# Optimization experiments

Measured on AMD Instinct MI355X. Metric: run time of the kernel, lower is better.

The kernel has to match this reference:

```python
import jax, jax.numpy as jnp
import numpy as np

B, T, D, H = 4, 2048, 1024, 16
HD = D // H


def setup_inputs() -> dict:
    key = jax.random.key(0)
    ks = jax.random.split(key, 9)
    s = 1.0 / np.sqrt(D)
    return {
        "x": jax.random.normal(ks[0], (B, T, D), dtype=jnp.float32),
        "Wq": jax.random.normal(ks[1], (D, D), dtype=jnp.float32) * s,
        "bq": jnp.zeros((D,), dtype=jnp.float32),
        "Wk": jax.random.normal(ks[2], (D, D), dtype=jnp.float32) * s,
        "bk": jnp.zeros((D,), dtype=jnp.float32),
        "Wv": jax.random.normal(ks[3], (D, D), dtype=jnp.float32) * s,
        "bv": jnp.zeros((D,), dtype=jnp.float32),
        "Wo": jax.random.normal(ks[4], (D, D), dtype=jnp.float32) * s,
        "bo": jnp.zeros((D,), dtype=jnp.float32),
    }


def reference(x, Wq, bq, Wk, bk, Wv, bv, Wo, bo):
    b, t, c = x.shape
    h, hd = H, HD
    scale = hd ** -0.5
    # projections: [B,T,C] -> [B,H,T,hd]
    q = (x @ Wq.T + bq).reshape(b, t, h, hd).transpose(0, 2, 1, 3)
    k = (x @ Wk.T + bk).reshape(b, t, h, hd).transpose(0, 2, 1, 3)
    v = (x @ Wv.T + bv).reshape(b, t, h, hd).transpose(0, 2, 1, 3)
    # scores [B,H,T,T], causal mask (no kv cache path, T > 1)
    attn = jnp.einsum("bhqd,bhkd->bhqk", q, k) * scale
    causal = jnp.triu(jnp.ones((t, t), dtype=bool), k=1)
    attn = jnp.where(causal, -jnp.inf, attn)
    attn = jax.nn.softmax(attn, axis=-1)
    out = jnp.einsum("bhqk,bhkd->bhqd", attn, v)
    out = out.transpose(0, 2, 1, 3).reshape(b, t, c)
    return (out @ Wo.T + bo, k, v)
```

## Files before the change

### kernel.cpp

```cpp
#include <hip/hip_runtime.h>
#include <hip/hip_bf16.h>
#include <cstdint>


typedef short bf16x8 __attribute__((ext_vector_type(8)));
typedef float f32x4 __attribute__((ext_vector_type(4)));

#define GLDS16(g, l)                                                          \
  __builtin_amdgcn_global_load_lds(                                           \
      (const __attribute__((address_space(1))) void*)(g),                     \
      (__attribute__((address_space(3))) void*)(l), 16, 0, 0)

static __device__ __forceinline__ short f2b(float f) {
  union { float f; unsigned u; } x; x.f = f;
  unsigned r = (x.u + 0x7FFFu + ((x.u >> 16) & 1u)) >> 16;
  return (short)r;
}

static __device__ __forceinline__ unsigned cvtpk2(float a, float b) {
  unsigned r;
  asm("v_cvt_pk_bf16_f32 %0, %1, %2" : "=v"(r) : "v"(a), "v"(b));
  return r;
}

__global__ void cvt_f32_bf16(const float* __restrict__ src, short* __restrict__ dst, int n4) {
  int i = blockIdx.x * blockDim.x + threadIdx.x;
  if (i < n4) {
    float4 v = ((const float4*)src)[i];
    short4 o; o.x = f2b(v.x); o.y = f2b(v.y); o.z = f2b(v.z); o.w = f2b(v.w);
    ((short4*)dst)[i] = o;
  }
}

__global__ void cvt_w4(const float* __restrict__ a, const float* __restrict__ b,
                       const float* __restrict__ c, const float* __restrict__ d,
                       short* __restrict__ dst) {
  int i = blockIdx.x * blockDim.x + threadIdx.x;
  int sel = i >> 18, j = i & 262143;
  const float* src = sel == 0 ? a : sel == 1 ? b : sel == 2 ? c : d;
  float4 v = ((const float4*)src)[j];
  short4 o; o.x = f2b(v.x); o.y = f2b(v.y); o.z = f2b(v.z); o.w = f2b(v.w);
  ((short4*)dst)[i] = o;
}

#define PIPE_STEP(BUF)                                                        \
  {                                                                          \
    asm volatile("s_waitcnt vmcnt(4) lgkmcnt(0)" ::: "memory");              \
    __builtin_amdgcn_s_barrier();                                            \
    __builtin_amdgcn_sched_barrier(0);                                       \
    stage((((BUF) + 2) % 3), (tile + 2) * 32);                               \
    compute(BUF);                                                            \
    ++tile;                                                                  \
  }

#define PIPE_TAIL()                                                          \
  asm volatile("s_waitcnt vmcnt(4) lgkmcnt(0)" ::: "memory");                \
  __builtin_amdgcn_s_barrier();                                              \
  __builtin_amdgcn_sched_barrier(0);                                         \
  compute(0);                                                   \
  asm volatile("s_waitcnt vmcnt(0) lgkmcnt(0)" ::: "memory");                \
  __builtin_amdgcn_s_barrier();                                              \
  __builtin_amdgcn_sched_barrier(0);                                         \
  compute(1);

__global__ __launch_bounds__(256) void gemm_qkv(
    const short* __restrict__ A,
    const short* __restrict__ W0, const short* __restrict__ W1, const short* __restrict__ W2,
    const float* __restrict__ b0, const float* __restrict__ b1, const float* __restrict__ b2,
    float* __restrict__ kf, float* __restrict__ vf,
    short* __restrict__ qbo, short* __restrict__ kbo, short* __restrict__ vtbo) {
  __shared__ short SM[24576];
  const int t = threadIdx.x;
  const int lane = t & 63;
  const int w = t >> 6;
  const int wm = w >> 1, wn = w & 1;
  const int quad = lane >> 4, l15 = lane & 15;
  const int bm = blockIdx.y;
  const int sel = blockIdx.x >> 3, bn = blockIdx.x & 7;
  const short* Bm = sel == 0 ? W0 : (sel == 1 ? W1 : W2);
  const float* bias = sel == 0 ? b0 : (sel == 1 ? b1 : b2);

  f32x4 acc[4][4];
  for (int i = 0; i < 4; i++)
    for (int j = 0; j < 4; j++) acc[i][j] = (f32x4){0.f, 0.f, 0.f, 0.f};

  const int c0 = t, c1 = t + 256;
  const int r0 = c0 >> 2, cc0 = c0 & 3;
  const int r1 = c1 >> 2, cc1 = c1 & 3;
  const short* Abase = A + (size_t)bm * 128 * 1024;
  const short* Bbase = Bm + (size_t)bn * 128 * 1024;

  auto stage = [&](int buf, int kk) {
    short* A_ = SM + buf * 4096;
    short* B_ = SM + 12288 + buf * 4096;
    GLDS16(Abase + (size_t)r0 * 1024 + kk + cc0 * 8, A_ + c0 * 8);
    GLDS16(Abase + (size_t)r1 * 1024 + kk + cc1 * 8, A_ + c1 * 8);
    GLDS16(Bbase + (size_t)r0 * 1024 + kk + cc0 * 8, B_ + c0 * 8);
    GLDS16(Bbase + (size_t)r1 * 1024 + kk + cc1 * 8, B_ + c1 * 8);
  };
  auto compute = [&](int buf) {
    const short* A_ = SM + buf * 4096;
    const short* B_ = SM + 12288 + buf * 4096;
    bf16x8 af[4], bfr[4];
    for (int mt = 0; mt < 4; mt++)
      af[mt] = *(const bf16x8*)(A_ + (wm * 64 + mt * 16 + l15) * 32 + quad * 8);
    for (int nt = 0; nt < 4; nt++)
      bfr[nt] = *(const bf16x8*)(B_ + (wn * 64 + nt * 16 + l15) * 32 + quad * 8);
    for (int mt = 0; mt < 4; mt++)
      for (int nt = 0; nt < 4; nt++)
        acc[mt][nt] = __builtin_amdgcn_mfma_f32_16x16x32_bf16(af[mt], bfr[nt], acc[mt][nt], 0, 0, 0);
  };

  stage(0, 0);
  stage(1, 32);
  int tile = 0;
  for (int ii = 0; ii < 10; ++ii) {
    PIPE_STEP(0) PIPE_STEP(1) PIPE_STEP(2)
  }
  PIPE_TAIL()

  if (sel != 2) {
    for (int mt = 0; mt < 4; mt++) {
      const int row_base = bm * 128 + wm * 64 + mt * 16 + quad * 4;
      for (int nt = 0; nt < 4; nt++) {
        const int col = bn * 128 + wn * 64 + nt * 16 + l15;
        const float bb = bias[col];
        for (int r = 0; r < 4; r++) {
          const int row = row_base + r;
          const float v = acc[mt][nt][r] + bb;
          const int b = row >> 11, tt = row & 2047;
          const int h = col >> 6, hi = col & 63;
          const size_t idx = (((size_t)(b * 16 + h)) * 2048 + tt) * 64 + hi;
          if (sel == 0) {
            qbo[idx] = f2b(v);
          } else {
            kf[idx] = v; kbo[idx] = f2b(v);
          }
        }
      }
    }
  } else {
    short* Tr = SM;
    __syncthreads();
    for (int mt = 0; mt < 4; mt++) {
      const int rowb = wm * 64 + mt * 16 + quad * 4;
      const int growb = bm * 128 + rowb;
      const int b_ = growb >> 11;
      for (int nt = 0; nt < 4; nt++) {
        const int colL = wn * 64 + nt * 16 + l15;
        const int col = bn * 128 + colL;
        const float bb = bias[col];
        const int h_ = col >> 6, hi_ = col & 63;
        short4 pk;
        for (int r = 0; r < 4; r++) {
          const float v = acc[mt][nt][r] + bb;
          const int tt = (growb + r) & 2047;
          vf[(((size_t)(b_ * 16 + h_)) * 2048 + tt) * 64 + hi_] = v;
          ((short*)&pk)[r] = f2b(v);
        }
        *(short4*)&Tr[colL * 136 + rowb] = pk;
      }
    }
    __syncthreads();
    const int c = t & 127, half = t >> 7;
    const int gcol = bn * 128 + c;
    const int h_ = gcol >> 6, hi_ = gcol & 63;
    for (int j = 0; j < 8; j++) {
      const int chunk = half * 8 + j;
      const int row0 = bm * 128 + chunk * 8;
      const int b_ = row0 >> 11, tt = row0 & 2047;
      bf16x8 val = *(const bf16x8*)&Tr[c * 136 + chunk * 8];
      *(bf16x8*)&vtbo[(((size_t)(b_ * 16 + h_)) * 64 + hi_) * 2048 + tt] = val;
    }
  }
}

__global__ __launch_bounds__(256) void gemm_o(
    const short* __restrict__ A, const short* __restrict__ Bm,
    const float* __restrict__ bias, float* __restrict__ out_f) {
  __shared__ short SM[24576];
  const int t = threadIdx.x;
  const int lane = t & 63;
  const int w = t >> 6;
  const int wm = w >> 1, wn = w & 1;
  const int quad = lane >> 4, l15 = lane & 15;
  const int bm = blockIdx.y, bn = blockIdx.x;

  f32x4 acc[4][4];
  for (int i = 0; i < 4; i++)
    for (int j = 0; j < 4; j++) acc[i][j] = (f32x4){0.f, 0.f, 0.f, 0.f};

  const int c0 = t, c1 = t + 256;
  const int r0 = c0 >> 2, cc0 = c0 & 3;
  const int r1 = c1 >> 2, cc1 = c1 & 3;
  const short* Abase = A + (size_t)bm * 128 * 1024;
  const short* Bbase = Bm + (size_t)bn * 128 * 1024;

  auto stage = [&](int buf, int kk) {
    short* A_ = SM + buf * 4096;
    short* B_ = SM + 12288 + buf * 4096;
    GLDS16(Abase + (size_t)r0 * 1024 + kk + cc0 * 8, A_ + c0 * 8);
    GLDS16(Abase + (size_t)r1 * 1024 + kk + cc1 * 8, A_ + c1 * 8);
    GLDS16(Bbase + (size_t)r0 * 1024 + kk + cc0 * 8, B_ + c0 * 8);
    GLDS16(Bbase + (size_t)r1 * 1024 + kk + cc1 * 8, B_ + c1 * 8);
  };
  auto compute = [&](int buf) {
    const short* A_ = SM + buf * 4096;
    const short* B_ = SM + 12288 + buf * 4096;
    bf16x8 af[4], bfr[4];
    for (int mt = 0; mt < 4; mt++)
      af[mt] = *(const bf16x8*)(A_ + (wm * 64 + mt * 16 + l15) * 32 + quad * 8);
    for (int nt = 0; nt < 4; nt++)
      bfr[nt] = *(const bf16x8*)(B_ + (wn * 64 + nt * 16 + l15) * 32 + quad * 8);
    for (int mt = 0; mt < 4; mt++)
      for (int nt = 0; nt < 4; nt++)
        acc[mt][nt] = __builtin_amdgcn_mfma_f32_16x16x32_bf16(af[mt], bfr[nt], acc[mt][nt], 0, 0, 0);
  };

  stage(0, 0);
  stage(1, 32);
  int tile = 0;
  for (int ii = 0; ii < 10; ++ii) {
    PIPE_STEP(0) PIPE_STEP(1) PIPE_STEP(2)
  }
  PIPE_TAIL()

  for (int mt = 0; mt < 4; mt++) {
    const int row_base = bm * 128 + wm * 64 + mt * 16 + quad * 4;
    for (int nt = 0; nt < 4; nt++) {
      const int col = bn * 128 + wn * 64 + nt * 16 + l15;
      const float bb = bias[col];
      for (int r = 0; r < 4; r++) {
        const int row = row_base + r;
        out_f[(size_t)row * 1024 + col] = acc[mt][nt][r] + bb;
      }
    }
  }
}

__global__ __launch_bounds__(256, 4) void attn_fwd(
    const short* __restrict__ Qb, const short* __restrict__ Kb,
    const short* __restrict__ VTb, short* __restrict__ Ob) {
  __shared__ short Ks[128 * 64];
  __shared__ short VTs[64 * 128];
  const int t = threadIdx.x;
  const int w = t >> 6;
  const int lane = t & 63;
  const int quad = lane >> 4, l15 = lane & 15;

  const int L = blockIdx.x + (blockIdx.y << 4);
  const int work = ((L & 7) << 7) + (L >> 3);
  const int bh = work >> 4;
  const int base = work & 15;
  const int b = bh >> 4, h = bh & 15;

  const short* Qh = Qb + (size_t)bh * 2048 * 64;
  const short* Kh = Kb + (size_t)bh * 2048 * 64;
  const short* VTh = VTb + (size_t)bh * 64 * 2048;
  unsigned* Pd = (unsigned*)Ks + w * 1024;
  const int swz = (l15 & 7) << 2;
  const float sscale = 0.125f * 1.4426950408889634f;

  for (int s = 0; s < 2; ++s) {
    const int qt = s ? (31 - base) : base;
    const int q0 = qt * 64 + w * 16;
    const bf16x8 qf0 = *(const bf16x8*)(Qh + (q0 + l15) * 64 + quad * 8);
    const bf16x8 qf1 = *(const bf16x8*)(Qh + (q0 + l15) * 64 + quad * 8 + 32);

    float m_q = -1e30f, l_q = 0.f;
    f32x4 o[4];
    for (int nt = 0; nt < 4; nt++) o[nt] = (f32x4){0.f, 0.f, 0.f, 0.f};
    const int ntile = (qt >> 1) + 1;

    for (int jt = 0; jt < ntile; ++jt) {
      const int j0 = jt << 7;
      __syncthreads();
      for (int rr = 0; rr < 4; rr++) {
        const int c = rr * 256 + t;
        const int row = c >> 3, colL = c & 7;
        const int colg = colL ^ (row & 7);
        GLDS16(Kh + (size_t)(j0 + row) * 64 + colg * 8, &Ks[c * 8]);
      }
      for (int rr = 0; rr < 4; rr++) {
        const int c = rr * 256 + t;
        const int row = c >> 4, colL = c & 15;
        const int colg = colL ^ (row & 7);
        GLDS16(VTh + (size_t)row * 2048 + j0 + colg * 8, &VTs[c * 8]);
      }
      __syncthreads();

      float sv[8][4];
      for (int si = 0; si < 8; ++si) {
        const int r = si * 16 + l15;
        bf16x8 kf0 = *(const bf16x8*)&Ks[(r * 8 + (quad ^ (r & 7))) * 8];
        bf16x8 kf1 = *(const bf16x8*)&Ks[(r * 8 + ((quad ^ 4) ^ (r & 7))) * 8];
        f32x4 z = (f32x4){0.f, 0.f, 0.f, 0.f};
        z = __builtin_amdgcn_mfma_f32_16x16x32_bf16(kf0, qf0, z, 0, 0, 0);
        z = __builtin_amdgcn_mfma_f32_16x16x32_bf16(kf1, qf1, z, 0, 0, 0);
        for (int r4 = 0; r4 < 4; r4++) sv[si][r4] = z[r4];
      }
      if (jt == ntile - 1) {
        const int qg = q0 + l15;
        for (int si = 0; si < 8; si++) {
          const int kbase = j0 + si * 16 + quad * 4;
          for (int r4 = 0; r4 < 4; r4++)
            if (kbase + r4 > qg) sv[si][r4] = -1e30f;
        }
      }
      float vmax = fmaxf(fmaxf(sv[0][0], sv[0][1]), fmaxf(sv[0][2], sv[0][3]));
      for (int si = 1; si < 8; si++) {
        float m2 = fmaxf(fmaxf(sv[si][0], sv[si][1]), fmaxf(sv[si][2], sv[si][3]));
        vmax = fmaxf(vmax, m2);
      }
      vmax = fmaxf(vmax, __shfl_xor(vmax, 16));
      vmax = fmaxf(vmax, __shfl_xor(vmax, 32));
      const float mn = fmaxf(m_q, vmax);
      if (__any(vmax > m_q)) {
        const float alpha = __builtin_amdgcn_exp2f((m_q - mn) * sscale);
        l_q *= alpha;
        float ar[4];
        for (int r4 = 0; r4 < 4; r4++) ar[r4] = __shfl(alpha, quad * 4 + r4);
        for (int nt = 0; nt < 4; nt++)
          for (int r4 = 0; r4 < 4; r4++) o[nt][r4] *= ar[r4];
      }
      m_q = mn;
      __syncthreads();

      const float negmns = -mn * sscale;
      float ssum = 0.f;
      for (int si = 0; si < 8; si++) {
        float p0 = __builtin_amdgcn_exp2f(fmaf(sv[si][0], sscale, negmns));
        float p1 = __builtin_amdgcn_exp2f(fmaf(sv[si][1], sscale, negmns));
        float p2 = __builtin_amdgcn_exp2f(fmaf(sv[si][2], sscale, negmns));
        float p3 = __builtin_amdgcn_exp2f(fmaf(sv[si][3], sscale, negmns));
        ssum += (p0 + p1) + (p2 + p3);
        uint2 pk; pk.x = cvtpk2(p0, p1); pk.y = cvtpk2(p2, p3);
        *(uint2*)(Pd + l15 * 64 + ((si * 8 + quad * 2) ^ swz)) = pk;
      }
      ssum += __shfl_xor(ssum, 16);
      ssum += __shfl_xor(ssum, 32);
      l_q += ssum;

      for (int kc = 0; kc < 4; kc++) {
        bf16x8 pf = *(const bf16x8*)(Pd + l15 * 64 + ((kc * 16 + quad * 4) ^ swz));
        for (int nt = 0; nt < 4; nt++) {
          const int rv = nt * 16 + l15;
          bf16x8 vf = *(const bf16x8*)&VTs[(rv * 16 + ((kc * 4 + quad) ^ (rv & 7))) * 8];
          o[nt] = __builtin_amdgcn_mfma_f32_16x16x32_bf16(pf, vf, o[nt], 0, 0, 0);
        }
      }
    }

    float lr[4], ri[4];
    for (int r4 = 0; r4 < 4; r4++) lr[r4] = __shfl(l_q, quad * 4 + r4);
    for (int r4 = 0; r4 < 4; r4++) ri[r4] = __builtin_amdgcn_rcpf(lr[r4]);
    for (int nt = 0; nt < 4; nt++) {
      const int col = h * 64 + nt * 16 + l15;
      for (int r4 = 0; r4 < 4; r4++) {
        const int q = q0 + quad * 4 + r4;
        Ob[((size_t)b * 2048 + q) * 1024 + col] = f2b(o[nt][r4] * ri[r4]);
      }
    }
  }
}

extern "C" void kernel_launch(void* const* d_in, const int* in_sizes, int n_in,
                              void* d_out, int out_size, void* d_ws, size_t ws_size,
                              hipStream_t stream) {
  const float* x  = (const float*)d_in[0];
  const float* Wq = (const float*)d_in[1];
  const float* bq = (const float*)d_in[2];
  const float* Wk = (const float*)d_in[3];
  const float* bk = (const float*)d_in[4];
  const float* Wv = (const float*)d_in[5];
  const float* bv = (const float*)d_in[6];
  const float* Wo = (const float*)d_in[7];
  const float* bo = (const float*)d_in[8];

  float* out   = (float*)d_out;
  float* k_out = out + (size_t)8388608;
  float* v_out = out + (size_t)16777216;

  short* ws  = (short*)d_ws;
  short* xb   = ws;
  short* wqb  = ws + 8388608;
  short* wkb  = ws + 9437184;
  short* wvb  = ws + 10485760;
  short* wob  = ws + 11534336;
  short* qb   = ws + 12582912;
  short* kb   = ws + 20971520;
  short* vtb  = ws + 29360128;
  short* attb = ws + 37748736;

  cvt_f32_bf16<<<8192, 256, 0, stream>>>(x, xb, 2097152);
  cvt_w4<<<4096, 256, 0, stream>>>(Wq, Wk, Wv, Wo, wqb);

  gemm_qkv<<<dim3(24, 64), 256, 0, stream>>>(
      xb, wqb, wkb, wvb, bq, bk, bv, k_out, v_out, qb, kb, vtb);

  attn_fwd<<<dim3(16, 64), 256, 0, stream>>>(qb, kb, vtb, attb);

  gemm_o<<<dim3(8, 64), 256, 0, stream>>>(attb, wob, bo, out);
}
```

Baseline: 328.6 us.

## Split K/V load waits with partial vmcnt barriers and vectorize output stores via LDS

Replaces the full __syncthreads with raw s_barrier plus explicit vmcnt waits. QK^T can now start once only the K tile has landed, while the V tile loads keep streaming until just before the PV MFMAs. The epilogue also stages each wave's normalized output in its LDS P buffer and writes 16-byte vectors to global memory instead of scattered 2-byte stores. The risk is correctness with raw barriers: the vmcnt counts must match the number of outstanding loads, and the LDS staging must not race with other waves.

```diff
diff --git a/kernel.cpp b/kernel.cpp
--- a/kernel.cpp
+++ b/kernel.cpp
@@ -274,7 +274,8 @@
 
     for (int jt = 0; jt < ntile; ++jt) {
       const int j0 = jt << 7;
-      __syncthreads();
+      __builtin_amdgcn_s_barrier();
+      __builtin_amdgcn_sched_barrier(0);
       for (int rr = 0; rr < 4; rr++) {
         const int c = rr * 256 + t;
         const int row = c >> 3, colL = c & 7;
@@ -287,7 +288,9 @@
         const int colg = colL ^ (row & 7);
         GLDS16(VTh + (size_t)row * 2048 + j0 + colg * 8, &VTs[c * 8]);
       }
-      __syncthreads();
+      asm volatile("s_waitcnt vmcnt(4)" ::: "memory");
+      __builtin_amdgcn_s_barrier();
+      __builtin_amdgcn_sched_barrier(0);
 
       float sv[8][4];
       for (int si = 0; si < 8; ++si) {
@@ -324,7 +327,8 @@
           for (int r4 = 0; r4 < 4; r4++) o[nt][r4] *= ar[r4];
       }
       m_q = mn;
-      __syncthreads();
+      __builtin_amdgcn_s_barrier();
+      __builtin_amdgcn_sched_barrier(0);
 
       const float negmns = -mn * sscale;
       float ssum = 0.f;
@@ -341,6 +345,10 @@
       ssum += __shfl_xor(ssum, 32);
       l_q += ssum;
 
+      asm volatile("s_waitcnt vmcnt(0)" ::: "memory");
+      __builtin_amdgcn_s_barrier();
+      __builtin_amdgcn_sched_barrier(0);
+
       for (int kc = 0; kc < 4; kc++) {
         bf16x8 pf = *(const bf16x8*)(Pd + l15 * 64 + ((kc * 16 + quad * 4) ^ swz));
         for (int nt = 0; nt < 4; nt++) {
@@ -354,12 +362,17 @@
     float lr[4], ri[4];
     for (int r4 = 0; r4 < 4; r4++) lr[r4] = __shfl(l_q, quad * 4 + r4);
     for (int r4 = 0; r4 < 4; r4++) ri[r4] = __builtin_amdgcn_rcpf(lr[r4]);
-    for (int nt = 0; nt < 4; nt++) {
-      const int col = h * 64 + nt * 16 + l15;
-      for (int r4 = 0; r4 < 4; r4++) {
-        const int q = q0 + quad * 4 + r4;
-        Ob[((size_t)b * 2048 + q) * 1024 + col] = f2b(o[nt][r4] * ri[r4]);
-      }
+    short* Po = (short*)Pd;
+    for (int nt = 0; nt < 4; nt++)
+      for (int r4 = 0; r4 < 4; r4++)
+        Po[(quad * 4 + r4) * 64 + nt * 16 + l15] = f2b(o[nt][r4] * ri[r4]);
+    asm volatile("s_waitcnt lgkmcnt(0)" ::: "memory");
+    __builtin_amdgcn_sched_barrier(0);
+    for (int k2 = 0; k2 < 2; k2++) {
+      const int F = lane + 64 * k2;
+      const int R = F >> 3, c = F & 7;
+      bf16x8 val = *(const bf16x8*)&Po[R * 64 + c * 8];
+      *(bf16x8*)&Ob[((size_t)(b * 2048 + q0 + R)) * 1024 + h * 64 + c * 8] = val;
     }
   }
 }
```

After: 324.3 us. About the same (-1.3%).

## Process paired causal query tiles together sharing K/V loads in attention

Applied to the files above, without the earlier changes.

The attention kernel moves to 512-thread blocks of 128 query rows, and each block handles two complementary query tiles (u and 15-u) in one pass over the K/V tiles. Each K/V tile staged in LDS is reused by both strips, which cuts global traffic and block-level syncs. P now gets its own LDS buffer with per-wave fences instead of a block barrier, and the output goes through LDS so it can be written with 16-byte stores. The costs are more registers (two accumulator sets), more LDS per block that may lower occupancy, and a new XCD-aware block-to-head mapping.

```diff
diff --git a/kernel.cpp b/kernel.cpp
--- a/kernel.cpp
+++ b/kernel.cpp
@@ -10,6 +10,12 @@
   __builtin_amdgcn_global_load_lds(                                           \
       (const __attribute__((address_space(1))) void*)(g),                     \
       (__attribute__((address_space(3))) void*)(l), 16, 0, 0)
+
+#define LDS_FENCE()                                                           \
+  do {                                                                        \
+    asm volatile("s_waitcnt lgkmcnt(0)" ::: "memory");                        \
+    __builtin_amdgcn_sched_barrier(0);                                        \
+  } while (0)
 
 static __device__ __forceinline__ short f2b(float f) {
   union { float f; unsigned u; } x; x.f = f;
@@ -238,57 +244,65 @@
   }
 }
 
-__global__ __launch_bounds__(256, 4) void attn_fwd(
+__global__ __launch_bounds__(512, 4) void attn_fwd(
     const short* __restrict__ Qb, const short* __restrict__ Kb,
     const short* __restrict__ VTb, short* __restrict__ Ob) {
   __shared__ short Ks[128 * 64];
   __shared__ short VTs[64 * 128];
+  __shared__ unsigned Ps[8 * 1024];
   const int t = threadIdx.x;
   const int w = t >> 6;
   const int lane = t & 63;
   const int quad = lane >> 4, l15 = lane & 15;
 
-  const int L = blockIdx.x + (blockIdx.y << 4);
-  const int work = ((L & 7) << 7) + (L >> 3);
-  const int bh = work >> 4;
-  const int base = work & 15;
+  const int xcd = blockIdx.x;
+  const int by = blockIdx.y;
+  const int bh = xcd * 8 + (by >> 3);
+  int u = by & 7; if (by & 32) u = 7 - u;
   const int b = bh >> 4, h = bh & 15;
+  const int qA = u, qB = 15 - u;
 
   const short* Qh = Qb + (size_t)bh * 2048 * 64;
   const short* Kh = Kb + (size_t)bh * 2048 * 64;
   const short* VTh = VTb + (size_t)bh * 64 * 2048;
-  unsigned* Pd = (unsigned*)Ks + w * 1024;
+  unsigned* Pw = Ps + w * 1024;
   const int swz = (l15 & 7) << 2;
   const float sscale = 0.125f * 1.4426950408889634f;
 
-  for (int s = 0; s < 2; ++s) {
-    const int qt = s ? (31 - base) : base;
-    const int q0 = qt * 64 + w * 16;
-    const bf16x8 qf0 = *(const bf16x8*)(Qh + (q0 + l15) * 64 + quad * 8);
-    const bf16x8 qf1 = *(const bf16x8*)(Qh + (q0 + l15) * 64 + quad * 8 + 32);
-
-    float m_q = -1e30f, l_q = 0.f;
-    f32x4 o[4];
-    for (int nt = 0; nt < 4; nt++) o[nt] = (f32x4){0.f, 0.f, 0.f, 0.f};
-    const int ntile = (qt >> 1) + 1;
-
-    for (int jt = 0; jt < ntile; ++jt) {
-      const int j0 = jt << 7;
-      __syncthreads();
-      for (int rr = 0; rr < 4; rr++) {
-        const int c = rr * 256 + t;
-        const int row = c >> 3, colL = c & 7;
-        const int colg = colL ^ (row & 7);
-        GLDS16(Kh + (size_t)(j0 + row) * 64 + colg * 8, &Ks[c * 8]);
-      }
-      for (int rr = 0; rr < 4; rr++) {
-        const int c = rr * 256 + t;
-        const int row = c >> 4, colL = c & 15;
-        const int colg = colL ^ (row & 7);
-        GLDS16(VTh + (size_t)row * 2048 + j0 + colg * 8, &VTs[c * 8]);
-      }
-      __syncthreads();
-
+  const int rA = qA * 128 + w * 16 + l15;
+  const int rB = qB * 128 + w * 16 + l15;
+  const bf16x8 qA0 = *(const bf16x8*)(Qh + (size_t)rA * 64 + quad * 8);
+  const bf16x8 qA1 = *(const bf16x8*)(Qh + (size_t)rA * 64 + quad * 8 + 32);
+  const bf16x8 qB0 = *(const bf16x8*)(Qh + (size_t)rB * 64 + quad * 8);
+  const bf16x8 qB1 = *(const bf16x8*)(Qh + (size_t)rB * 64 + quad * 8 + 32);
+
+  float mA = -1e30f, lA = 0.f, mB = -1e30f, lB = 0.f;
+  f32x4 oA[4], oB[4];
+  for (int nt = 0; nt < 4; nt++) {
+    oA[nt] = (f32x4){0.f, 0.f, 0.f, 0.f};
+    oB[nt] = (f32x4){0.f, 0.f, 0.f, 0.f};
+  }
+
+  const int ntile = 16 - u;
+  for (int jt = 0; jt < ntile; ++jt) {
+    const int j0 = jt << 7;
+    __syncthreads();
+    for (int rr = 0; rr < 2; rr++) {
+      const int c = rr * 512 + t;
+      const int row = c >> 3, colL = c & 7;
+      const int colg = colL ^ (row & 7);
+      GLDS16(Kh + (size_t)(j0 + row) * 64 + colg * 8, &Ks[c * 8]);
+    }
+    for (int rr = 0; rr < 2; rr++) {
+      const int c = rr * 512 + t;
+      const int row = c >> 4, colL = c & 15;
+      const int colg = colL ^ (row & 7);
+      GLDS16(VTh + (size_t)row * 2048 + j0 + colg * 8, &VTs[c * 8]);
+    }
+    __syncthreads();
+
+    auto strip = [&](const bf16x8& qf0, const bf16x8& qf1, int qg, bool diag,
+                     float& m_q, float& l_q, f32x4* o) {
       float sv[8][4];
       for (int si = 0; si < 8; ++si) {
         const int r = si * 16 + l15;
@@ -299,8 +313,7 @@
         z = __builtin_amdgcn_mfma_f32_16x16x32_bf16(kf1, qf1, z, 0, 0, 0);
         for (int r4 = 0; r4 < 4; r4++) sv[si][r4] = z[r4];
       }
-      if (jt == ntile - 1) {
-        const int qg = q0 + l15;
+      if (diag) {
         for (int si = 0; si < 8; si++) {
           const int kbase = j0 + si * 16 + quad * 4;
           for (int r4 = 0; r4 < 4; r4++)
@@ -324,8 +337,6 @@
           for (int r4 = 0; r4 < 4; r4++) o[nt][r4] *= ar[r4];
       }
       m_q = mn;
-      __syncthreads();
-
       const float negmns = -mn * sscale;
       float ssum = 0.f;
       for (int si = 0; si < 8; si++) {
@@ -335,33 +346,47 @@
         float p3 = __builtin_amdgcn_exp2f(fmaf(sv[si][3], sscale, negmns));
         ssum += (p0 + p1) + (p2 + p3);
         uint2 pk; pk.x = cvtpk2(p0, p1); pk.y = cvtpk2(p2, p3);
-        *(uint2*)(Pd + l15 * 64 + ((si * 8 + quad * 2) ^ swz)) = pk;
+        *(uint2*)(Pw + l15 * 64 + ((si * 8 + quad * 2) ^ swz)) = pk;
       }
       ssum += __shfl_xor(ssum, 16);
       ssum += __shfl_xor(ssum, 32);
       l_q += ssum;
-
+      LDS_FENCE();
       for (int kc = 0; kc < 4; kc++) {
-        bf16x8 pf = *(const bf16x8*)(Pd + l15 * 64 + ((kc * 16 + quad * 4) ^ swz));
+        bf16x8 pf = *(const bf16x8*)(Pw + l15 * 64 + ((kc * 16 + quad * 4) ^ swz));
         for (int nt = 0; nt < 4; nt++) {
           const int rv = nt * 16 + l15;
           bf16x8 vf = *(const bf16x8*)&VTs[(rv * 16 + ((kc * 4 + quad) ^ (rv & 7))) * 8];
           o[nt] = __builtin_amdgcn_mfma_f32_16x16x32_bf16(pf, vf, o[nt], 0, 0, 0);
         }
       }
-    }
-
+      LDS_FENCE();
+    };
+
+    strip(qB0, qB1, rB, jt == ntile - 1, mB, lB, oB);
+    if (jt <= u) strip(qA0, qA1, rA, jt == u, mA, lA, oA);
+  }
+
+  auto epi = [&](float l_q, const f32x4* o, int qp) {
     float lr[4], ri[4];
     for (int r4 = 0; r4 < 4; r4++) lr[r4] = __shfl(l_q, quad * 4 + r4);
     for (int r4 = 0; r4 < 4; r4++) ri[r4] = __builtin_amdgcn_rcpf(lr[r4]);
-    for (int nt = 0; nt < 4; nt++) {
-      const int col = h * 64 + nt * 16 + l15;
-      for (int r4 = 0; r4 < 4; r4++) {
-        const int q = q0 + quad * 4 + r4;
-        Ob[((size_t)b * 2048 + q) * 1024 + col] = f2b(o[nt][r4] * ri[r4]);
-      }
-    }
-  }
+    short* Po = (short*)Pw;
+    LDS_FENCE();
+    for (int nt = 0; nt < 4; nt++)
+      for (int r4 = 0; r4 < 4; r4++)
+        Po[(quad * 4 + r4) * 64 + nt * 16 + l15] = f2b(o[nt][r4] * ri[r4]);
+    LDS_FENCE();
+    const int q0 = qp * 128 + w * 16;
+    for (int k2 = 0; k2 < 2; k2++) {
+      const int F = lane + 64 * k2;
+      const int R = F >> 3, c = F & 7;
+      bf16x8 val = *(const bf16x8*)&Po[R * 64 + c * 8];
+      *(bf16x8*)&Ob[((size_t)(b * 2048 + q0 + R)) * 1024 + h * 64 + c * 8] = val;
+    }
+  };
+  epi(lB, oB, qB);
+  epi(lA, oA, qA);
 }
 
 extern "C" void kernel_launch(void* const* d_in, const int* in_sizes, int n_in,
@@ -398,7 +423,7 @@
   gemm_qkv<<<dim3(24, 64), 256, 0, stream>>>(
       xb, wqb, wkb, wvb, bq, bk, bv, k_out, v_out, qb, kb, vtb);
 
-  attn_fwd<<<dim3(16, 64), 256, 0, stream>>>(qb, kb, vtb, attb);
+  attn_fwd<<<dim3(8, 64), 512, 0, stream>>>(qb, kb, vtb, attb);
 
   gemm_o<<<dim3(8, 64), 256, 0, stream>>>(attb, wob, bo, out);
 }
```

Result: slower. 364.3 us (+10.8%).
